# Kernel optimization log

Hardware: AMD Instinct MI355X
Metric: run time of the kernel (lower is better)

Reference implementation:

```python
import jax, jax.numpy as jnp
import numpy as np

B, L, S = 128, 80, 8          # dialogues, utterances per dialogue, speakers
NODE_DIM, HIDDEN, HEADS, OUT_DIM = 768, 512, 8, 256
N = B * L


def _build_edges():
    """Replicates InterSentenceGNN.build_graph + Batch.from_data_list offsets."""
    rel = np.zeros((N, 3), np.float32)
    all_e, last = [], []
    eye3 = np.eye(3, dtype=np.float32)
    for b in range(B):
        off = b * L
        u = L - 1
        e, t = [], []
        for i in range(L):
            if i > 0:
                e += [[i - 1, i], [i, i - 1]]; t += [0, 0]   # REL_SEQ
            if i < u:
                e += [[i, u], [u, i]]; t += [1, 1]           # REL_CTX
        for s in range(S):                                   # REL_SPK, round-robin speakers
            g = list(range(s, L, S))
            for a in range(len(g)):
                for c in range(a + 1, len(g)):
                    e += [[g[a], g[c]], [g[c], g[a]]]; t += [2, 2]
        e = np.asarray(e, np.int64); t = np.asarray(t, np.int64)
        np.add.at(rel, e[:, 0] + off, eye3[t])               # out-degree per relation (pre-unique)
        all_e.append(np.unique(e, axis=0) + off)             # torch.unique(idx, dim=1)
        last.append(off + u)
    edge_index = np.concatenate(all_e, 0).T.astype(np.int32)  # [2, E], row0=src, row1=dst
    return edge_index, rel, np.asarray(last, np.int32)


def setup_inputs() -> dict:
    key = jax.random.key(0)
    ks = jax.random.split(key, 16)
    edge_index, rel_feat, last_idx = _build_edges()
    g = lambda k, shp, fan: jax.random.normal(k, shp, jnp.float32) * (1.0 / np.sqrt(fan))
    return {
        "x": jax.random.normal(ks[0], (N, NODE_DIM), jnp.float32),
        "rel_feat": jnp.asarray(rel_feat),
        "w1": g(ks[1], (3, 64), 3), "b1": jnp.zeros((64,), jnp.float32),
        "w2": g(ks[2], (64, 1), 64), "b2": jnp.zeros((1,), jnp.float32),
        "Wl1": g(ks[3], (NODE_DIM, HIDDEN), NODE_DIM), "bl1": jnp.zeros((HIDDEN,), jnp.float32),
        "Wr1": g(ks[4], (NODE_DIM, HIDDEN), NODE_DIM), "br1": jnp.zeros((HIDDEN,), jnp.float32),
        "att1": g(ks[5], (HEADS, HIDDEN // HEADS), HIDDEN // HEADS),
        "bias1": jnp.zeros((HIDDEN,), jnp.float32),
        "Wl2": g(ks[6], (HIDDEN, OUT_DIM), HIDDEN), "bl2": jnp.zeros((OUT_DIM,), jnp.float32),
        "Wr2": g(ks[7], (HIDDEN, OUT_DIM), HIDDEN), "br2": jnp.zeros((OUT_DIM,), jnp.float32),
        "att2": g(ks[8], (1, OUT_DIM), OUT_DIM),
        "bias2": jnp.zeros((OUT_DIM,), jnp.float32),
        "ln_g": jnp.ones((OUT_DIM,), jnp.float32), "ln_b": jnp.zeros((OUT_DIM,), jnp.float32),
        "edge_index": jnp.asarray(edge_index),
        "last_idx": jnp.asarray(last_idx),
    }


def _gatv2(x, Wl, bl, Wr, br, att, bias, src, dst, heads, ch, concat):
    """PyG GATv2Conv (eval mode, self-loops already in src/dst)."""
    n = x.shape[0]
    xl = (x @ Wl + bl).reshape(n, heads, ch)   # source transform (messages)
    xr = (x @ Wr + br).reshape(n, heads, ch)   # target transform
    e = jax.nn.leaky_relu(xl[src] + xr[dst], negative_slope=0.2)  # [E,H,C]
    logit = jnp.einsum("ehc,hc->eh", e, att)                      # [E,H]
    m = jax.ops.segment_max(logit, dst, num_segments=n)
    a = jnp.exp(logit - m[dst])
    denom = jax.ops.segment_sum(a, dst, num_segments=n)
    alpha = a / denom[dst]                                        # segment softmax over dst
    msg = (xl[src] * alpha[:, :, None]).reshape(-1, heads * ch)
    out = jax.ops.segment_sum(msg, dst, num_segments=n).reshape(n, heads, ch)
    out = out.reshape(n, heads * ch) if concat else out.mean(axis=1)
    return out + bias


def reference(x, rel_feat, w1, b1, w2, b2, Wl1, bl1, Wr1, br1, att1, bias1,
              Wl2, bl2, Wr2, br2, att2, bias2, ln_g, ln_b, edge_index, last_idx):
    n = x.shape[0]
    loops = jnp.arange(n, dtype=edge_index.dtype)
    src = jnp.concatenate([edge_index[0], loops])  # add_self_loops=True (PyG default)
    dst = jnp.concatenate([edge_index[1], loops])
    w = jax.nn.sigmoid(jax.nn.relu(rel_feat @ w1 + b1) @ w2 + b2)  # [N,1] node gate
    h = x * w
    h = jax.nn.elu(_gatv2(h, Wl1, bl1, Wr1, br1, att1, bias1, src, dst, HEADS, HIDDEN // HEADS, True))
    h = _gatv2(h, Wl2, bl2, Wr2, br2, att2, bias2, src, dst, 1, OUT_DIM, False)
    mu = jnp.mean(h, axis=-1, keepdims=True)
    var = jnp.mean((h - mu) ** 2, axis=-1, keepdims=True)
    h = (h - mu) * jax.lax.rsqrt(var + 1e-5) * ln_g + ln_b
    return h[last_idx]  # x[batch.ptr[1:] - 1]: last (context) node per dialogue
```

## Files before the change

kernel.cpp:

```cpp
#include <hip/hip_runtime.h>
#include <hip/hip_bf16.h>

#define NN 10240
#define LL 80
#define BB 128

typedef _Float16 half8 __attribute__((ext_vector_type(8)));
typedef _Float16 half2v __attribute__((ext_vector_type(2)));
typedef float f32x4 __attribute__((ext_vector_type(4)));

#define GLD16(gptr, lptr)                                                        \
  __builtin_amdgcn_global_load_lds(                                              \
      (const __attribute__((address_space(1))) void*)(gptr),                     \
      (__attribute__((address_space(3))) void*)(lptr), 16, 0, 0)

__device__ __forceinline__ float dot2f(half2v a, half2v b, float c) {
#if __has_builtin(__builtin_amdgcn_fdot2)
  return __builtin_amdgcn_fdot2(a, b, c, false);
#else
  return c + (float)a.x * (float)b.x + (float)a.y * (float)b.y;
#endif
}
__device__ __forceinline__ half2v u2h(unsigned int u) { half2v r; __builtin_memcpy(&r, &u, 4); return r; }
__device__ __forceinline__ unsigned int h2u(half2v h) { unsigned int u; __builtin_memcpy(&u, &h, 4); return u; }
__device__ __forceinline__ int roff(int r) { return r * 72; }

__device__ __forceinline__ float dotq4r(uint4 a, uint4 b, const half2v* atv, int qb, float acc) {
  const half2v c02 = {(_Float16)0.2f, (_Float16)0.2f};
  unsigned int aa[4] = {a.x, a.y, a.z, a.w};
  unsigned int bb[4] = {b.x, b.y, b.z, b.w};
#pragma unroll
  for (int j = 0; j < 4; ++j) {
    half2v e = u2h(aa[j]) + u2h(bb[j]);
    half2v l = __builtin_elementwise_max(e, e * c02);
    acc = dot2f(l, atv[qb + j], acc);
  }
  return acc;
}

__global__ __launch_bounds__(256) void prep_all(
    const float* __restrict__ x, const float* __restrict__ rel,
    const float* __restrict__ w1, const float* __restrict__ b1,
    const float* __restrict__ w2, const float* __restrict__ b2,
    const float* __restrict__ Wl1, const float* __restrict__ Wr1,
    const float* __restrict__ Wl2, const float* __restrict__ Wr2,
    const float* __restrict__ bl1, const float* __restrict__ br1,
    const float* __restrict__ att1,
    _Float16* __restrict__ h0, _Float16* __restrict__ Wt1,
    _Float16* __restrict__ Wt2cat,
    float* __restrict__ biasc, _Float16* __restrict__ att_h) {
  __shared__ float tile[32][33];
  int bid = blockIdx.x;
  int tid = threadIdx.x;
  if (bid < NN) {
    int n = bid;
    __shared__ float s_w;
    if (tid < 64) {
      float r0 = rel[n * 3 + 0], r1 = rel[n * 3 + 1], r2 = rel[n * 3 + 2];
      float v = r0 * w1[tid] + r1 * w1[64 + tid] + r2 * w1[128 + tid] + b1[tid];
      v = v > 0.f ? v : 0.f;
      v *= w2[tid];
      for (int d = 32; d; d >>= 1) v += __shfl_down(v, d, 64);
      if (tid == 0) s_w = 1.f / (1.f + __expf(-(v + b2[0])));
    }
    __syncthreads();
    float w = s_w;
    const float* xr = x + (size_t)n * 768;
    _Float16* hr = h0 + (size_t)n * 768;
    for (int c = tid; c < 768; c += 256) hr[c] = (_Float16)(xr[c] * w);
    return;
  }
  int r = bid - NN;
  const float* W;
  _Float16* Wt;
  int K, Nc, bx, by;
  if (r < 384)      { W = Wl1; Wt = Wt1;                          K = 768; Nc = 512; bx = r % 16;       by = r / 16; }
  else if (r < 768) { W = Wr1; Wt = Wt1 + (size_t)512 * 768;      K = 768; Nc = 512; bx = (r-384) % 16; by = (r-384) / 16; }
  else if (r < 896) { W = Wl2; Wt = Wt2cat;                       K = 512; Nc = 256; bx = (r-768) % 8;  by = (r-768) / 8; }
  else if (r < 1024){ W = Wr2; Wt = Wt2cat + (size_t)256 * 512;   K = 512; Nc = 256; bx = (r-896) % 8;  by = (r-896) / 8; }
  else {
    for (int i = tid; i < 1024; i += 256) biasc[i] = (i < 512) ? bl1[i] : br1[i - 512];
    for (int i = tid; i < 512; i += 256) att_h[i] = (_Float16)att1[i];
    return;
  }
  int n0 = bx * 32, k0 = by * 32;
  int c = tid & 31, rr = tid >> 5;
#pragma unroll
  for (int p = 0; p < 4; ++p) {
    int rw = p * 8 + rr;
    tile[rw][c] = W[(size_t)(k0 + rw) * Nc + n0 + c];
  }
  __syncthreads();
#pragma unroll
  for (int p = 0; p < 4; ++p) {
    int rw = p * 8 + rr;
    Wt[(size_t)(n0 + rw) * K + k0 + c] = (_Float16)tile[c][rw];
  }
}

__global__ __launch_bounds__(512, 8) void gemm1gat1(
    const _Float16* __restrict__ h0, const _Float16* __restrict__ Wt1,
    const float* __restrict__ biasc, const _Float16* __restrict__ att_h,
    const float* __restrict__ bias1, _Float16* __restrict__ h1) {
  __shared__ __align__(16) char smem[39936];
  _Float16* As = (_Float16*)smem;
  _Float16* Bs = (_Float16*)(smem + 15360);
  _Float16* s_xl = (_Float16*)smem;
  _Float16* s_xr = (_Float16*)(smem + 11520);
  float* s_logit = (float*)(smem + 23040);
  signed char* s_src8 = (signed char*)(smem + 27200);
  float* s_hub = (float*)(smem + 28240);
  _Float16* s_xlT = (_Float16*)(smem + 28560);
  _Float16* s_P = (_Float16*)smem;

  int bx = blockIdx.x;
  int h = bx >> 7, b = bx & 127;
  int base = b * LL;
  int tid = threadIdx.x;
  int wave = tid >> 6, lane = tid & 63;
  int lr = lane & 15, lk = lane >> 4;

  int seg8 = ((lane & 3) ^ ((lane >> 3) & 3)) * 8;
  const _Float16* aP = h0;
  if (wave < 5) {
    int c = wave * 64 + lane;
    aP = h0 + (size_t)(base + (c >> 2)) * 768 + seg8;
  }
  int cB = wave * 64 + lane;
  int brow = cB >> 2;
  int wrow = (brow < 64) ? (h * 64 + brow) : (512 + h * 64 + (brow - 64));
  const _Float16* bP = Wt1 + (size_t)wrow * 768 + seg8;
  int xk8 = (lk ^ ((lr >> 1) & 3)) * 8;

  f32x4 acc[5] = {};
  for (int it = 0; it < 8; ++it) {
    int k0 = it * 96;
    if (wave < 5) {
      GLD16(aP + k0,      As + wave * 512);
      GLD16(aP + k0 + 32, As + 2560 + wave * 512);
      GLD16(aP + k0 + 64, As + 5120 + wave * 512);
    }
    GLD16(bP + k0,      Bs + wave * 512);
    GLD16(bP + k0 + 32, Bs + 4096 + wave * 512);
    GLD16(bP + k0 + 64, Bs + 8192 + wave * 512);
    __syncthreads();
#pragma unroll
    for (int s3 = 0; s3 < 3; ++s3) {
      half8 bf = *(const half8*)(Bs + s3 * 4096 + (wave * 16 + lr) * 32 + xk8);
#pragma unroll
      for (int m = 0; m < 5; ++m) {
        half8 af = *(const half8*)(As + s3 * 2560 + (m * 16 + lr) * 32 + xk8);
        acc[m] = __builtin_amdgcn_mfma_f32_16x16x32_f16(af, bf, acc[m], 0, 0, 0);
      }
    }
    __syncthreads();
  }
  {
    int c = wave * 16 + lr;
    bool isxl = c < 64;
    int cc = isxl ? c : c - 64;
    float bb = biasc[(isxl ? 0 : 512) + h * 64 + cc];
    _Float16* dst = isxl ? s_xl : s_xr;
#pragma unroll
    for (int m = 0; m < 5; ++m)
#pragma unroll
      for (int rg = 0; rg < 4; ++rg) {
        int row = m * 16 + lk * 4 + rg;
        _Float16 hv = (_Float16)(acc[m][rg] + bb);
        dst[roff(row) + cc] = hv;
        if (isxl) s_xlT[cc * 88 + row] = hv;
      }
  }
  if (tid < 79) {
    int d = tid;
    signed char list[13];
    int c = 0;
    list[c++] = (signed char)d;
    if (d > 0) list[c++] = (signed char)(d - 1);
    if (d + 1 < 79) list[c++] = (signed char)(d + 1);
    list[c++] = 79;
    for (int j = d & 7; j < 80; j += 8)
      if (j != d && j != 79) list[c++] = (signed char)j;
    for (int i = c; i < 13; ++i) list[i] = -1;
#pragma unroll
    for (int i = 0; i < 13; ++i) s_src8[i * 80 + d] = list[i];
  }
  __syncthreads();

  const unsigned int* pat = (const unsigned int*)(att_h + h * 64);
  half2v atv[32];
#pragma unroll
  for (int q = 0; q < 32; ++q) atv[q] = u2h(__builtin_amdgcn_readfirstlane(pat[q]));
  if (tid < 474) {
    int d = tid / 6, io = tid % 6;
    const uint4* pxr = (const uint4*)(s_xr + roff(d));
    uint4 xrr[8];
#pragma unroll
    for (int q = 0; q < 8; ++q) xrr[q] = pxr[q];
#pragma unroll
    for (int k = 0; k < 3; ++k) {
      int i = io + 6 * k;
      if (i < 13) {
        int src = s_src8[i * 80 + d];
        if (src < 0) {
          s_logit[i * 80 + d] = -3e38f;
        } else {
          const uint4* pxl = (const uint4*)(s_xl + roff(src));
          float a2 = 0.f;
#pragma unroll
          for (int q = 0; q < 8; ++q) a2 = dotq4r(pxl[q], xrr[q], atv, q * 4, a2);
          s_logit[i * 80 + d] = a2;
        }
      }
    }
  } else {
    int j = tid - 474;
    const uint4* pxr = (const uint4*)(s_xr + roff(79));
    uint4 xrr[8];
#pragma unroll
    for (int q = 0; q < 8; ++q) xrr[q] = pxr[q];
#pragma unroll
    for (int k = 0; k < 3; ++k) {
      int s = j + 38 * k;
      if (s < 80) {
        const uint4* pxl = (const uint4*)(s_xl + roff(s));
        float a2 = 0.f;
#pragma unroll
        for (int q = 0; q < 8; ++q) a2 = dotq4r(pxl[q], xrr[q], atv, q * 4, a2);
        s_hub[s] = a2;
      }
    }
  }
  __syncthreads();

  {
    uint4 z4 = {0u, 0u, 0u, 0u};
    for (int z = tid; z < 1040; z += 512) ((uint4*)smem)[z] = z4;
  }
  float va[13], inv_d = 0.f;
  bool isd = tid < 79;
  if (isd) {
    int d = tid;
    float m = -3e38f;
#pragma unroll
    for (int i = 0; i < 13; ++i) { va[i] = s_logit[i * 80 + d]; m = fmaxf(m, va[i]); }
    float sum = 0.f;
#pragma unroll
    for (int i = 0; i < 13; ++i) { va[i] = __expf(va[i] - m); sum += va[i]; }
    inv_d = 1.f / sum;
  }
  float he0 = 0.f, he1 = 0.f, hinv = 0.f;
  if (wave == 7) {
    int l = lane;
    float v0 = s_hub[l];
    float v1 = (l < 16) ? s_hub[64 + l] : -3e38f;
    float m = fmaxf(v0, v1);
    for (int d = 32; d; d >>= 1) m = fmaxf(m, __shfl_xor(m, d, 64));
    he0 = __expf(v0 - m);
    he1 = (l < 16) ? __expf(v1 - m) : 0.f;
    float sum = he0 + he1;
    for (int d = 32; d; d >>= 1) sum += __shfl_xor(sum, d, 64);
    hinv = 1.f / sum;
  }
  __syncthreads();

  if (isd) {
    int d = tid;
#pragma unroll
    for (int i = 0; i < 13; ++i) {
      int src = s_src8[i * 80 + d];
      if (src >= 0) s_P[d * 104 + src] = (_Float16)(va[i] * inv_d);
    }
  }
  if (wave == 7) {
    int l = lane;
    s_P[79 * 104 + l] = (_Float16)(he0 * hinv);
    if (l < 16) s_P[79 * 104 + 64 + l] = (_Float16)(he1 * hinv);
  }
  __syncthreads();

  {
    int nt = (wave < 4) ? 3 : 2;
    int tb = (wave < 4) ? wave * 3 : 12 + (wave - 4) * 2;
    for (int tt = 0; tt < nt; ++tt) {
      int t = tb + tt;
      int m = t >> 2, n = t & 3;
      f32x4 a = {};
#pragma unroll
      for (int kc = 0; kc < 3; ++kc) {
        half8 af = *(const half8*)(s_P + (m * 16 + lr) * 104 + kc * 32 + lk * 8);
        half8 bf = *(const half8*)(s_xlT + (n * 16 + lr) * 88 + kc * 32 + lk * 8);
        a = __builtin_amdgcn_mfma_f32_16x16x32_f16(af, bf, a, 0, 0, 0);
      }
      int c = n * 16 + lr;
      float bb = bias1[h * 64 + c];
#pragma unroll
      for (int rg = 0; rg < 4; ++rg) {
        int d = m * 16 + lk * 4 + rg;
        float v = a[rg] + bb;
        v = v > 0.f ? v : __expf(v) - 1.f;
        h1[(size_t)(base + d) * 512 + h * 64 + c] = (_Float16)v;
      }
    }
  }
}

#define PX 266
__global__ __launch_bounds__(512) void gemm2gat2(
    const _Float16* __restrict__ h1, const _Float16* __restrict__ Bt,
    const float* __restrict__ bl2, const float* __restrict__ br2,
    const float* __restrict__ att2, const float* __restrict__ bias2,
    const float* __restrict__ ln_g, const float* __restrict__ ln_b,
    float* __restrict__ out) {
  __shared__ __align__(16) char smem[80 * PX * 2];
  __shared__ _Float16 s_att[256];
  __shared__ _Float16 s_xr[256];
  __shared__ float s_red[80];
  __shared__ float s_sum[4], s_sq[4];
  _Float16* As = (_Float16*)smem;
  _Float16* Bs = (_Float16*)(smem + 5120);
  _Float16* s_x = (_Float16*)smem;

  int b = blockIdx.x;
  int tid = threadIdx.x;
  int wave = tid >> 6, lane = tid & 63;
  int lr = lane & 15, lk = lane >> 4;

  if (tid < 256) s_att[tid] = (_Float16)att2[tid];

  int seg8 = ((lane & 3) ^ ((lane >> 3) & 3)) * 8;
  int achunk = wave * 64 + lane;
  const _Float16* aP = h1 + (size_t)(b * 80 + (achunk >> 2)) * 512 + seg8;
  const _Float16* bP0 = Bt + (size_t)((wave * 128 + lane) >> 2) * 512 + seg8;
  const _Float16* bP1 = Bt + (size_t)((wave * 128 + 64 + lane) >> 2) * 512 + seg8;
  int xk8 = (lk ^ ((lr >> 1) & 3)) * 8;
  f32x4 acc[5][2] = {};
  for (int k0 = 0; k0 < 512; k0 += 32) {
    if (wave < 5) GLD16(aP + k0, As + wave * 512);
    GLD16(bP0 + k0, Bs + (wave * 128) * 8);
    GLD16(bP1 + k0, Bs + (wave * 128 + 64) * 8);
    __syncthreads();
    half8 af[5];
#pragma unroll
    for (int i = 0; i < 5; ++i)
      af[i] = *(const half8*)(As + (i * 16 + lr) * 32 + xk8);
#pragma unroll
    for (int j = 0; j < 2; ++j) {
      half8 bfv = *(const half8*)(Bs + ((wave * 2 + j) * 16 + lr) * 32 + xk8);
#pragma unroll
      for (int i = 0; i < 5; ++i)
        acc[i][j] = __builtin_amdgcn_mfma_f32_16x16x32_f16(af[i], bfv, acc[i][j], 0, 0, 0);
    }
    __syncthreads();
  }
#pragma unroll
  for (int i = 0; i < 5; ++i)
#pragma unroll
    for (int j = 0; j < 2; ++j)
#pragma unroll
      for (int rg = 0; rg < 4; ++rg) {
        int row = i * 16 + lk * 4 + rg;
        int col = (wave * 2 + j) * 16 + lr;
        s_x[row * PX + col] = (_Float16)(acc[i][j][rg] + bl2[col]);
      }
  {
    int c = tid >> 1, kh = tid & 1;
    const uint4* wr = (const uint4*)(Bt + (size_t)(256 + c) * 512 + kh * 256);
    const uint4* hq = (const uint4*)(h1 + (size_t)(b * 80 + 79) * 512 + kh * 256);
    float s = 0.f;
#pragma unroll 8
    for (int q = 0; q < 32; ++q) {
      uint4 ua = hq[q], uw = wr[q];
      s = dot2f(u2h(ua.x), u2h(uw.x), s);
      s = dot2f(u2h(ua.y), u2h(uw.y), s);
      s = dot2f(u2h(ua.z), u2h(uw.z), s);
      s = dot2f(u2h(ua.w), u2h(uw.w), s);
    }
    s += __shfl_xor(s, 1, 64);
    if (kh == 0) s_xr[c] = (_Float16)(s + br2[c]);
  }
  __syncthreads();
  if (tid < 160) {
    int r = tid >> 1, hf = tid & 1;
    const half2v* xa = (const half2v*)(s_x + r * PX + hf * 128);
    const half2v* xr = (const half2v*)(s_xr + hf * 128);
    const half2v* at = (const half2v*)(s_att + hf * 128);
    float lg = 0.f;
    const half2v c02 = {(_Float16)0.2f, (_Float16)0.2f};
#pragma unroll
    for (int q = 0; q < 64; ++q) {
      half2v e = xa[q] + xr[q];
      half2v l = __builtin_elementwise_max(e, e * c02);
      lg = dot2f(l, at[q], lg);
    }
    lg += __shfl_xor(lg, 1, 64);
    if (hf == 0) s_red[r] = lg;
  }
  __syncthreads();
  if (wave == 7) {
    float v0 = s_red[lane];
    float v1 = (lane < 16) ? s_red[64 + lane] : -3e38f;
    float m = fmaxf(v0, v1);
    for (int d = 32; d; d >>= 1) m = fmaxf(m, __shfl_xor(m, d, 64));
    float e0 = __expf(v0 - m);
    float e1 = (lane < 16) ? __expf(v1 - m) : 0.f;
    float sum = e0 + e1;
    for (int d = 32; d; d >>= 1) sum += __shfl_xor(sum, d, 64);
    float inv = 1.f / sum;
    s_red[lane] = e0 * inv;
    if (lane < 16) s_red[64 + lane] = e1 * inv;
  }
  __syncthreads();
  float v = 0.f;
  if (tid < 256) {
    float a = 0.f;
#pragma unroll
    for (int r = 0; r < 80; ++r) a += s_red[r] * (float)s_x[r * PX + tid];
    v = a + bias2[tid];
    float p = v;
    for (int d = 32; d; d >>= 1) p += __shfl_down(p, d, 64);
    if (lane == 0) s_sum[wave] = p;
    float q = v * v;
    for (int d = 32; d; d >>= 1) q += __shfl_down(q, d, 64);
    if (lane == 0) s_sq[wave] = q;
  }
  __syncthreads();
  if (tid < 256) {
    float mu = (s_sum[0] + s_sum[1] + s_sum[2] + s_sum[3]) * (1.f / 256.f);
    float ex2 = (s_sq[0] + s_sq[1] + s_sq[2] + s_sq[3]) * (1.f / 256.f);
    float var = ex2 - mu * mu;
    float r = rsqrtf(var + 1e-5f);
    out[b * 256 + tid] = (v - mu) * r * ln_g[tid] + ln_b[tid];
  }
}

extern "C" void kernel_launch(void* const* d_in, const int* in_sizes, int n_in,
                              void* d_out, int out_size, void* d_ws, size_t ws_size,
                              hipStream_t stream) {
  const float* x      = (const float*)d_in[0];
  const float* rel    = (const float*)d_in[1];
  const float* w1     = (const float*)d_in[2];
  const float* b1     = (const float*)d_in[3];
  const float* w2     = (const float*)d_in[4];
  const float* b2     = (const float*)d_in[5];
  const float* Wl1    = (const float*)d_in[6];
  const float* bl1    = (const float*)d_in[7];
  const float* Wr1    = (const float*)d_in[8];
  const float* br1    = (const float*)d_in[9];
  const float* att1   = (const float*)d_in[10];
  const float* bias1  = (const float*)d_in[11];
  const float* Wl2    = (const float*)d_in[12];
  const float* bl2    = (const float*)d_in[13];
  const float* Wr2    = (const float*)d_in[14];
  const float* br2    = (const float*)d_in[15];
  const float* att2   = (const float*)d_in[16];
  const float* bias2  = (const float*)d_in[17];
  const float* ln_g   = (const float*)d_in[18];
  const float* ln_b   = (const float*)d_in[19];
  float* out = (float*)d_out;

  char* p = (char*)d_ws;
  _Float16* h0     = (_Float16*)p; p += (size_t)NN * 768 * 2;
  _Float16* h1     = (_Float16*)p; p += (size_t)NN * 512 * 2;
  _Float16* Wt1    = (_Float16*)p; p += (size_t)1024 * 768 * 2;
  _Float16* Wt2cat = (_Float16*)p; p += (size_t)512 * 512 * 2;
  _Float16* att_h  = (_Float16*)p; p += 1024;
  float* biasc     = (float*)p; p += 1024 * 4;

  prep_all<<<NN + 1025, 256, 0, stream>>>(x, rel, w1, b1, w2, b2, Wl1, Wr1, Wl2, Wr2,
                                          bl1, br1, att1, h0, Wt1, Wt2cat, biasc, att_h);

  gemm1gat1<<<1024, 512, 0, stream>>>(h0, Wt1, biasc, att_h, bias1, h1);

  gemm2gat2<<<BB, 512, 0, stream>>>(h1, Wt2cat, bl2, br2, att2, bias2, ln_g, ln_b, out);
}
```

Measured before the change: 182.2 us.

## Double-buffer LDS K-tiles in both GEMM+GAT kernels to overlap loads with MFMA

Measured after the change: 186.8 us. +2.6%, slower.

```diff
diff --git a/kernel.cpp b/kernel.cpp
--- a/kernel.cpp
+++ b/kernel.cpp
@@ -98,13 +98,13 @@
   }
 }
 
-__global__ __launch_bounds__(512, 8) void gemm1gat1(
+__global__ __launch_bounds__(512, 6) void gemm1gat1(
     const _Float16* __restrict__ h0, const _Float16* __restrict__ Wt1,
     const float* __restrict__ biasc, const _Float16* __restrict__ att_h,
     const float* __restrict__ bias1, _Float16* __restrict__ h1) {
-  __shared__ __align__(16) char smem[39936];
-  _Float16* As = (_Float16*)smem;
-  _Float16* Bs = (_Float16*)(smem + 15360);
+  __shared__ __align__(16) char smem[53248];
+  _Float16* Ab = (_Float16*)smem;
+  _Float16* Bb = (_Float16*)(smem + 20480);
   _Float16* s_xl = (_Float16*)smem;
   _Float16* s_xr = (_Float16*)(smem + 11520);
   float* s_logit = (float*)(smem + 23040);
@@ -120,36 +120,50 @@
   int wave = tid >> 6, lane = tid & 63;
   int lr = lane & 15, lk = lane >> 4;
 
-  int seg8 = ((lane & 3) ^ ((lane >> 3) & 3)) * 8;
-  const _Float16* aP = h0;
+  int segA8 = ((lane & 7) ^ ((lane >> 3) & 7)) * 8;
+  int r0a = wave * 16 + (lane >> 3);
+  const _Float16* aP0 = h0;
+  const _Float16* aP1 = h0;
   if (wave < 5) {
-    int c = wave * 64 + lane;
-    aP = h0 + (size_t)(base + (c >> 2)) * 768 + seg8;
-  }
-  int cB = wave * 64 + lane;
-  int brow = cB >> 2;
-  int wrow = (brow < 64) ? (h * 64 + brow) : (512 + h * 64 + (brow - 64));
-  const _Float16* bP = Wt1 + (size_t)wrow * 768 + seg8;
-  int xk8 = (lk ^ ((lr >> 1) & 3)) * 8;
+    aP0 = h0 + (size_t)(base + r0a) * 768 + segA8;
+    aP1 = h0 + (size_t)(base + r0a + 8) * 768 + segA8;
+  }
+  int rb0 = r0a, rb1 = r0a + 8;
+  int wr0 = (rb0 < 64) ? (h * 64 + rb0) : (512 + h * 64 + (rb0 - 64));
+  int wr1 = (rb1 < 64) ? (h * 64 + rb1) : (512 + h * 64 + (rb1 - 64));
+  const _Float16* bP0 = Wt1 + (size_t)wr0 * 768 + segA8;
+  const _Float16* bP1 = Wt1 + (size_t)wr1 * 768 + segA8;
 
   f32x4 acc[5] = {};
-  for (int it = 0; it < 8; ++it) {
-    int k0 = it * 96;
-    if (wave < 5) {
-      GLD16(aP + k0,      As + wave * 512);
-      GLD16(aP + k0 + 32, As + 2560 + wave * 512);
-      GLD16(aP + k0 + 64, As + 5120 + wave * 512);
-    }
-    GLD16(bP + k0,      Bs + wave * 512);
-    GLD16(bP + k0 + 32, Bs + 4096 + wave * 512);
-    GLD16(bP + k0 + 64, Bs + 8192 + wave * 512);
-    __syncthreads();
-#pragma unroll
-    for (int s3 = 0; s3 < 3; ++s3) {
-      half8 bf = *(const half8*)(Bs + s3 * 4096 + (wave * 16 + lr) * 32 + xk8);
+  if (wave < 5) {
+    GLD16(aP0, Ab + wave * 1024);
+    GLD16(aP1, Ab + wave * 1024 + 512);
+  }
+  GLD16(bP0, Bb + wave * 1024);
+  GLD16(bP1, Bb + wave * 1024 + 512);
+  __syncthreads();
+  for (int t = 0; t < 12; ++t) {
+    int cur = t & 1;
+    if (t < 11) {
+      int k0 = (t + 1) * 64;
+      int nb = cur ^ 1;
+      if (wave < 5) {
+        GLD16(aP0 + k0, Ab + nb * 5120 + wave * 1024);
+        GLD16(aP1 + k0, Ab + nb * 5120 + wave * 1024 + 512);
+      }
+      GLD16(bP0 + k0, Bb + nb * 8192 + wave * 1024);
+      GLD16(bP1 + k0, Bb + nb * 8192 + wave * 1024 + 512);
+    }
+    const _Float16* Ac = Ab + cur * 5120;
+    const _Float16* Bc = Bb + cur * 8192;
+    int rB = wave * 16 + lr;
+#pragma unroll
+    for (int s2 = 0; s2 < 2; ++s2) {
+      int cx = ((s2 * 4 + lk) ^ (lr & 7)) * 8;
+      half8 bf = *(const half8*)(Bc + rB * 64 + cx);
 #pragma unroll
       for (int m = 0; m < 5; ++m) {
-        half8 af = *(const half8*)(As + s3 * 2560 + (m * 16 + lr) * 32 + xk8);
+        half8 af = *(const half8*)(Ac + (m * 16 + lr) * 64 + cx);
         acc[m] = __builtin_amdgcn_mfma_f32_16x16x32_f16(af, bf, acc[m], 0, 0, 0);
       }
     }
@@ -312,13 +326,13 @@
     const float* __restrict__ att2, const float* __restrict__ bias2,
     const float* __restrict__ ln_g, const float* __restrict__ ln_b,
     float* __restrict__ out) {
-  __shared__ __align__(16) char smem[80 * PX * 2];
+  __shared__ __align__(16) char smem[43008];
   __shared__ _Float16 s_att[256];
   __shared__ _Float16 s_xr[256];
   __shared__ float s_red[80];
   __shared__ float s_sum[4], s_sq[4];
-  _Float16* As = (_Float16*)smem;
-  _Float16* Bs = (_Float16*)(smem + 5120);
+  _Float16* Ab = (_Float16*)smem;
+  _Float16* Bb = (_Float16*)(smem + 10240);
   _Float16* s_x = (_Float16*)smem;
 
   int b = blockIdx.x;
@@ -335,18 +349,28 @@
   const _Float16* bP1 = Bt + (size_t)((wave * 128 + 64 + lane) >> 2) * 512 + seg8;
   int xk8 = (lk ^ ((lr >> 1) & 3)) * 8;
   f32x4 acc[5][2] = {};
-  for (int k0 = 0; k0 < 512; k0 += 32) {
-    if (wave < 5) GLD16(aP + k0, As + wave * 512);
-    GLD16(bP0 + k0, Bs + (wave * 128) * 8);
-    GLD16(bP1 + k0, Bs + (wave * 128 + 64) * 8);
-    __syncthreads();
+  if (wave < 5) GLD16(aP, Ab + wave * 512);
+  GLD16(bP0, Bb + wave * 1024);
+  GLD16(bP1, Bb + wave * 1024 + 512);
+  __syncthreads();
+  for (int t = 0; t < 16; ++t) {
+    int cur = t & 1;
+    if (t < 15) {
+      int k0 = (t + 1) * 32;
+      int nb = cur ^ 1;
+      if (wave < 5) GLD16(aP + k0, Ab + nb * 2560 + wave * 512);
+      GLD16(bP0 + k0, Bb + nb * 8192 + wave * 1024);
+      GLD16(bP1 + k0, Bb + nb * 8192 + wave * 1024 + 512);
+    }
+    const _Float16* Ac = Ab + cur * 2560;
+    const _Float16* Bc = Bb + cur * 8192;
     half8 af[5];
 #pragma unroll
     for (int i = 0; i < 5; ++i)
-      af[i] = *(const half8*)(As + (i * 16 + lr) * 32 + xk8);
+      af[i] = *(const half8*)(Ac + (i * 16 + lr) * 32 + xk8);
 #pragma unroll
     for (int j = 0; j < 2; ++j) {
-      half8 bfv = *(const half8*)(Bs + ((wave * 2 + j) * 16 + lr) * 32 + xk8);
+      half8 bfv = *(const half8*)(Bc + ((wave * 2 + j) * 16 + lr) * 32 + xk8);
 #pragma unroll
       for (int i = 0; i < 5; ++i)
         acc[i][j] = __builtin_amdgcn_mfma_f32_16x16x32_f16(af[i], bfv, acc[i][j], 0, 0, 0);
```
